# Kernel tuning notes

Hardware: AMD Instinct MI355X
Metric: run time of the kernel (lower is better)

## Reference

```python
import jax, jax.numpy as jnp
import numpy as np

E = 1024
BUCKET = 16
TAU = 0.75
ITERS = 8
SCALE = E ** -0.5
EPS = 1e-6


def _gumbel(rng, shape):
    u = jax.random.uniform(rng, shape, jnp.float32, 0.0, 1.0)
    return -jnp.log(-jnp.log(u + EPS) + EPS)


def _log_sinkhorn(log_alpha, n_iter):
    def body(i, la):
        la = la - jax.scipy.special.logsumexp(la, axis=-1, keepdims=True)
        la = la - jax.scipy.special.logsumexp(la, axis=-2, keepdims=True)
        return la
    return jnp.exp(jax.lax.fori_loop(0, n_iter, body, log_alpha))


def setup_inputs() -> dict:
    rng = jax.random.key(0)
    ks = jax.random.split(rng, 9)
    T, B, S = 4096, 8, 4096
    w = 0.02
    return {
        "query": jax.random.normal(ks[0], (T, B, E), jnp.float32),
        "key": jax.random.normal(ks[1], (S, B, E), jnp.float32),
        "value": jax.random.normal(ks[2], (S, B, E), jnp.float32),
        "wq": jax.random.normal(ks[3], (E, E), jnp.float32) * w,
        "bq": jnp.zeros((E,), jnp.float32),
        "wk": jax.random.normal(ks[4], (E, E), jnp.float32) * w,
        "bk": jnp.zeros((E,), jnp.float32),
        "wo": jax.random.normal(ks[5], (E, E), jnp.float32) * w,
        "bo": jnp.zeros((E,), jnp.float32),
    }


def reference(query, key, value, wq, bq, wk, bk, wo, bo):
    T, B, _ = query.shape
    S = key.shape[0]
    # projections (Linear: x @ W.T + b), move to (B, T, E)
    q = jnp.einsum('tbe,fe->btf', query, wq) + bq
    k = jnp.einsum('sbe,fe->bsf', key, wk) + bk
    v = jnp.transpose(value, (1, 0, 2))  # (B, S, E)
    nb, nkb = T // BUCKET, S // BUCKET
    # bucket aggregation: mean-pool q/k, flatten v buckets
    qb = q.reshape(B, nb, BUCKET, E).mean(axis=2)          # (B, nb, E)
    kb = k.reshape(B, nkb, BUCKET, E).mean(axis=2)         # (B, nkb, E)
    vb = v.reshape(B, nkb, BUCKET * E)                     # (B, nkb, BUCKET*E)
    # dot energy
    logits = jnp.einsum('bqe,bke->bqk', qb, kb) * SCALE    # (B, nb, nkb)
    log_alpha = logits
    # gumbel-sinkhorn (noise=True)
    g = _gumbel(jax.random.key(42), logits.shape)
    attn_weights = _log_sinkhorn((logits.astype(jnp.float32) + g) / TAU, ITERS)
    # attend on flattened buckets, then un-aggregate
    attn = jnp.einsum('bqk,bkd->bqd', attn_weights, vb)    # (B, nb, BUCKET*E)
    attn = attn.reshape(B, nb * BUCKET, E)
    attn = jnp.transpose(attn, (1, 0, 2))                  # (T, B, E)
    out = jnp.einsum('tbe,fe->tbf', attn, wo) + bo
    return out, attn_weights, log_alpha
```

## Files before the change

### kernel.cpp

```cpp
#include <hip/hip_runtime.h>


typedef float    f32x4 __attribute__((ext_vector_type(4)));
typedef _Float16 h4    __attribute__((ext_vector_type(4)));
typedef _Float16 h8    __attribute__((ext_vector_type(8)));

#define OUT_ELEMS 33554432
#define AW_ELEMS  524288

__device__ __forceinline__ void gload16(const void* g, void* l) {
  __builtin_amdgcn_global_load_lds((__attribute__((address_space(1))) void*)g,
                                   (__attribute__((address_space(3))) void*)l,
                                   16, 0, 0);
}

__global__ __launch_bounds__(256) void cb_k(const float* __restrict__ wq,
                                            const float* __restrict__ wk,
                                            const float* __restrict__ wo,
                                            _Float16* __restrict__ wdst,
                                            const float* __restrict__ q,
                                            const float* __restrict__ k,
                                            _Float16* __restrict__ qbar,
                                            _Float16* __restrict__ kbar) {
  __shared__ __attribute__((aligned(16))) float ldsbuf[16384];
  int bid = blockIdx.x;
  int tid = threadIdx.x;
  if (bid < 3072) {
    int which = bid >> 10;
    const float* src = which == 0 ? wq : (which == 1 ? wk : wo);
    size_t idx = (size_t)(bid & 1023) * 256 + tid;
    f32x4 v = ((const f32x4*)src)[idx];
    ((h4*)(wdst + (size_t)which * 1048576))[idx] = __builtin_convertvector(v, h4);
  } else {
    int vb = bid - 3072;
    int srcid = vb >> 11;
    int rem = vb & 2047;
    int i = rem >> 3;
    int b = (rem + i) & 7;
    const float* s2 = srcid ? k : q;
    _Float16* d2 = srcid ? kbar : qbar;
    const int w = tid >> 6;
    #pragma unroll
    for (int j = 0; j < 16; ++j) {
      int row = (i * 16 + j) * 8 + b;
      gload16(s2 + (size_t)row * 1024 + tid * 4, &ldsbuf[j * 1024 + w * 256]);
    }
    __syncthreads();
    const f32x4* l4 = (const f32x4*)ldsbuf;
    f32x4 a = {0.f, 0.f, 0.f, 0.f};
    #pragma unroll
    for (int j = 0; j < 16; ++j) a += l4[j * 256 + tid];
    a *= 0.0625f;
    ((h4*)(d2 + (size_t)(b * 256 + i) * 1024))[tid] = __builtin_convertvector(a, h4);
  }
}

__device__ __forceinline__ unsigned rotl32(unsigned x, int r) {
  return (x << r) | (x >> (32 - r));
}
__global__ __launch_bounds__(256) void gumbel_k(const float* __restrict__ logits,
                                                float* __restrict__ ebuf) {
  unsigned i = blockIdx.x * 256 + threadIdx.x;
  const unsigned k0 = 0u, k1 = 42u, k2 = 0u ^ 42u ^ 0x1BD11BDAu;
  unsigned x0 = 0u + k0, x1 = i + k1;
#define R4(a,b,c,d) \
  x0 += x1; x1 = rotl32(x1, a); x1 ^= x0; \
  x0 += x1; x1 = rotl32(x1, b); x1 ^= x0; \
  x0 += x1; x1 = rotl32(x1, c); x1 ^= x0; \
  x0 += x1; x1 = rotl32(x1, d); x1 ^= x0;
  R4(13,15,26,6)  x0 += k1; x1 += k2 + 1u;
  R4(17,29,16,24) x0 += k2; x1 += k0 + 2u;
  R4(13,15,26,6)  x0 += k0; x1 += k1 + 3u;
  R4(17,29,16,24) x0 += k1; x1 += k2 + 4u;
  R4(13,15,26,6)  x0 += k2; x1 += k0 + 5u;
#undef R4
  unsigned bits = x0 ^ x1;
  float u = __builtin_bit_cast(float, (bits >> 9) | 0x3f800000u) - 1.0f;
  float g = -logf(-logf(u + 1e-6f) + 1e-6f);
  ebuf[i] = __expf((logits[i] + g) / 0.75f);
}

__global__ __launch_bounds__(1024) void sinkvt_k(const float* __restrict__ ein,
                                                 float* __restrict__ attnw,
                                                 _Float16* __restrict__ wsh,
                                                 const float* __restrict__ v,
                                                 _Float16* __restrict__ vt) {
  __shared__ __attribute__((aligned(16))) char smem[36864];
  const int t = threadIdx.x;
  if (blockIdx.x < 8) {
    const int b = blockIdx.x;
    const int r = t >> 2, p = t & 3;
    const int k = t & 255, g = t >> 8;
    const float* Eb = ein + (size_t)b * 65536;
    const f32x4* Eb4 = (const f32x4*)Eb;
    float* ra = (float*)smem;
    float* cb = ra + 256;
    float (*part)[256] = (float (*)[256])(cb + 256);
    if (t < 256) cb[t] = 1.0f;
    __syncthreads();
    const f32x4* cb4 = (const f32x4*)cb;

    for (int it = 0; it < 8; ++it) {
      float s = 0.f;
      #pragma unroll
      for (int i = 0; i < 16; ++i) {
        f32x4 e = Eb4[r * 64 + p * 16 + i];
        f32x4 c = cb4[p * 16 + i];
        f32x4 m = e * c;
        s += (m[0] + m[1]) + (m[2] + m[3]);
      }
      s += __shfl_xor(s, 1, 64);
      s += __shfl_xor(s, 2, 64);
      if (p == 0) ra[r] = 1.0f / s;
      __syncthreads();
      float s2 = 0.f;
      #pragma unroll 8
      for (int q2 = 0; q2 < 64; ++q2) {
        int row = g * 64 + q2;
        s2 += Eb[row * 256 + k] * ra[row];
      }
      part[g][k] = s2;
      __syncthreads();
      if (t < 256) {
        cb[t] = 1.0f / (part[0][t] + part[1][t] + part[2][t] + part[3][t]);
      }
      __syncthreads();
    }

    const float arow = ra[r];
    f32x4* aw = (f32x4*)(attnw + (size_t)b * 65536 + r * 256 + p * 64);
    h4* wh = (h4*)(wsh + (size_t)b * 65536 + r * 256 + p * 64);
    #pragma unroll
    for (int i = 0; i < 16; ++i) {
      f32x4 e = Eb4[r * 64 + p * 16 + i];
      f32x4 c = cb4[p * 16 + i];
      f32x4 w = e * c * arow;
      aw[i] = w;
      h4 hv;
      hv[0] = (_Float16)w[0]; hv[1] = (_Float16)w[1];
      hv[2] = (_Float16)w[2]; hv[3] = (_Float16)w[3];
      wh[i] = hv;
    }
  } else {
    const int s = t >> 8, t2 = t & 255;
    int bid = (blockIdx.x - 8) * 4 + s;
    _Float16 (*tile)[72] = (_Float16 (*)[72])(smem + s * 9216);
    int kb = bid & 3, eb = (bid >> 2) & 15, j = (bid >> 6) & 15;
    int b = ((bid >> 10) + (bid & 7)) & 7;
    int k0 = kb * 64, e0 = eb * 64;
    int r = t2 >> 2, qq = t2 & 3;
    const float* src = v + ((size_t)((k0 + r) * 16 + j) * 8 + b) * 1024 + e0;
    #pragma unroll
    for (int ii = 0; ii < 4; ++ii) {
      f32x4 x = ((const f32x4*)src)[qq + ii * 4];
      *(h4*)&tile[r][(qq + ii * 4) * 4] = __builtin_convertvector(x, h4);
    }
    __syncthreads();
    _Float16* dstp = vt + (((size_t)(b * 16 + j) * 1024 + e0 + r) * 256 + k0 + qq * 16);
    h8 o0, o1;
    #pragma unroll
    for (int kk = 0; kk < 8; ++kk) o0[kk] = tile[qq * 16 + kk][r];
    #pragma unroll
    for (int kk = 0; kk < 8; ++kk) o1[kk] = tile[qq * 16 + 8 + kk][r];
    *(h8*)dstp = o0;
    *(h8*)(dstp + 8) = o1;
  }
}

template <int MODE>
__global__ __launch_bounds__(256) void gemm128(const _Float16* __restrict__ A,
                                               const _Float16* __restrict__ B,
                                               const float* __restrict__ bias,
                                               const float* __restrict__ bias2,
                                               void* __restrict__ out0,
                                               int K, int lda, int ldb) {
  const int tid = threadIdx.x, lane = tid & 63, w = tid >> 6;
  int bx = blockIdx.x, by = blockIdx.y, bz = blockIdx.z;
  if constexpr (MODE == 0) {
    int wid = ((bx & 7) << 4) + (bx >> 3);
    by = wid & 7; bx = wid >> 3;
  }
  if constexpr (MODE == 2) {
    int wid = ((bx & 7) << 8) + (bx >> 3);
    bz = wid >> 4; by = (wid >> 1) & 7; bx = wid & 1;
  }
  if constexpr (MODE == 3) {
    int wid = ((bx & 7) << 8) + (bx >> 3);
    by = wid & 7; bx = wid >> 3;
  }
  const int m0 = bx * 128, n0 = by * 128;
  const _Float16* Ab = A;
  const _Float16* Bb = B;
  const float* bs = bias;
  if constexpr (MODE == 0) {
    Ab += (size_t)bz * 2097152;
    Bb += (size_t)bz * 1048576;
    if (bz) bs = bias2;
  }
  if constexpr (MODE == 1) { Ab += (size_t)bz * 262144; Bb += (size_t)bz * 262144; }
  if constexpr (MODE == 2) { Ab += (size_t)(bz >> 4) * 65536; Bb += (size_t)bz * 262144; }
  __shared__ _Float16 lA[128 * 32];
  __shared__ _Float16 lB[128 * 32];
  f32x4 acc[4][4] = {};
  const int wm = (w >> 1) * 64, wn = (w & 1) * 64;
  const int fr = lane & 15, fk = (lane >> 4) * 8;
  const int q0 = tid, q1 = tid + 256;

  for (int kt = 0; kt < K; kt += 32) {
    __syncthreads();
    gload16(Ab + (size_t)(m0 + (q0 >> 2)) * lda + kt + (q0 & 3) * 8, &lA[(w * 64) * 8]);
    gload16(Ab + (size_t)(m0 + (q1 >> 2)) * lda + kt + (q1 & 3) * 8, &lA[(256 + w * 64) * 8]);
    gload16(Bb + (size_t)(n0 + (q0 >> 2)) * ldb + kt + (q0 & 3) * 8, &lB[(w * 64) * 8]);
    gload16(Bb + (size_t)(n0 + (q1 >> 2)) * ldb + kt + (q1 & 3) * 8, &lB[(256 + w * 64) * 8]);
    __syncthreads();
    h8 af[4], bf[4];
    #pragma unroll
    for (int i = 0; i < 4; ++i) {
      af[i] = *(const h8*)&lA[(wm + i * 16 + fr) * 32 + fk];
      bf[i] = *(const h8*)&lB[(wn + i * 16 + fr) * 32 + fk];
    }
    #pragma unroll
    for (int mi = 0; mi < 4; ++mi)
      #pragma unroll
      for (int ni = 0; ni < 4; ++ni)
        acc[mi][ni] = __builtin_amdgcn_mfma_f32_16x16x32_f16(af[mi], bf[ni], acc[mi][ni], 0, 0, 0);
  }

  const int er = (lane >> 4) * 4;
  #pragma unroll
  for (int mi = 0; mi < 4; ++mi) {
    #pragma unroll
    for (int ni = 0; ni < 4; ++ni) {
      #pragma unroll
      for (int r = 0; r < 4; ++r) {
        int row = m0 + wm + mi * 16 + er + r;
        int col = n0 + wn + ni * 16 + fr;
        float val = acc[mi][ni][r];
        if constexpr (MODE == 0) {
          ((_Float16*)out0)[(size_t)bz * 2097152 + (size_t)row * 1024 + col] =
              (_Float16)(val + bs[col]);
        } else if constexpr (MODE == 1) {
          ((float*)out0)[(size_t)bz * 65536 + row * 256 + col] = val * 0.03125f;
        } else if constexpr (MODE == 2) {
          int b = bz >> 4, j = bz & 15;
          ((_Float16*)out0)[((size_t)(b * 4096 + row * 16 + j)) * 1024 + col] = (_Float16)val;
        } else {
          int bb = row >> 12, t = row & 4095;
          ((float*)out0)[((size_t)t * 8 + bb) * 1024 + col] = val + bs[col];
        }
      }
    }
  }
}

extern "C" void kernel_launch(void* const* d_in, const int* in_sizes, int n_in,
                              void* d_out, int out_size, void* d_ws, size_t ws_size,
                              hipStream_t stream) {
  const float* query = (const float*)d_in[0];
  const float* key   = (const float*)d_in[1];
  const float* value = (const float*)d_in[2];
  const float* wq    = (const float*)d_in[3];
  const float* bq    = (const float*)d_in[4];
  const float* wk    = (const float*)d_in[5];
  const float* bk    = (const float*)d_in[6];
  const float* wo    = (const float*)d_in[7];
  const float* bo    = (const float*)d_in[8];

  float* out      = (float*)d_out;
  float* attnw    = out + OUT_ELEMS;
  float* logalpha = out + OUT_ELEMS + AW_ELEMS;

  char* ws = (char*)d_ws;
  const size_t MB = 1024 * 1024;
  _Float16* wqh   = (_Float16*)(ws + 0 * MB);
  _Float16* woh   = (_Float16*)(ws + 4 * MB);
  _Float16* qbar  = (_Float16*)(ws + 6 * MB);
  _Float16* kbar  = (_Float16*)(ws + 10 * MB);
  _Float16* qbh   = (_Float16*)(ws + 14 * MB);
  _Float16* kbh   = (_Float16*)(ws + 18 * MB);
  float*    ebuf  = (float*)(ws + 22 * MB);
  _Float16* wsh   = (_Float16*)(ws + 25 * MB);
  _Float16* vt    = (_Float16*)(ws + 26 * MB);
  _Float16* attnh = (_Float16*)(ws + 90 * MB);
  (void)in_sizes; (void)n_in; (void)out_size; (void)ws_size;

  cb_k<<<dim3(7168), 256, 0, stream>>>(wq, wk, wo, wqh, query, key, qbar, kbar);

  gemm128<0><<<dim3(128, 1, 2), 256, 0, stream>>>(qbar, wqh, bq, bk, qbh, 1024, 1024, 1024);
  gemm128<1><<<dim3(2, 2, 8), 256, 0, stream>>>(qbh, kbh, nullptr, nullptr, logalpha, 1024, 1024, 1024);

  gumbel_k<<<dim3(2048), 256, 0, stream>>>(logalpha, ebuf);
  sinkvt_k<<<dim3(2056), 1024, 0, stream>>>(ebuf, attnw, wsh, value, vt);

  gemm128<2><<<dim3(2048), 256, 0, stream>>>(wsh, vt, nullptr, nullptr, attnh, 256, 256, 256);
  gemm128<3><<<dim3(2048), 256, 0, stream>>>(attnh, woh, bo, nullptr, out, 1024, 1024, 1024);
}
```

Before: 345.9 us.

## Replace output projection GEMM with 256x256-tile double-buffered MFMA kernel

The final output projection (32768x1024x1024) moves from the generic 128x128 gemm to a dedicated 512-thread kernel with 256x256 tiles and a K-step of 64. Operands are staged with global_load_lds into a double buffer in 128KB of dynamic LDS, and the wait counts and barriers are arranged so the next tile's loads overlap the MFMA work. The larger tile raises arithmetic intensity and cuts global traffic per FLOP, at the cost of one block per CU, fewer blocks (512), and possible LDS bank conflicts from the unpadded layout.

```diff
diff --git a/kernel.cpp b/kernel.cpp
--- a/kernel.cpp
+++ b/kernel.cpp
@@ -184,10 +184,6 @@
     int wid = ((bx & 7) << 8) + (bx >> 3);
     bz = wid >> 4; by = (wid >> 1) & 7; bx = wid & 1;
   }
-  if constexpr (MODE == 3) {
-    int wid = ((bx & 7) << 8) + (bx >> 3);
-    by = wid & 7; bx = wid >> 3;
-  }
   const int m0 = bx * 128, n0 = by * 128;
   const _Float16* Ab = A;
   const _Float16* Bb = B;
@@ -241,13 +237,98 @@
               (_Float16)(val + bs[col]);
         } else if constexpr (MODE == 1) {
           ((float*)out0)[(size_t)bz * 65536 + row * 256 + col] = val * 0.03125f;
-        } else if constexpr (MODE == 2) {
+        } else {
           int b = bz >> 4, j = bz & 15;
           ((_Float16*)out0)[((size_t)(b * 4096 + row * 16 + j)) * 1024 + col] = (_Float16)val;
-        } else {
-          int bb = row >> 12, t = row & 4095;
-          ((float*)out0)[((size_t)t * 8 + bb) * 1024 + col] = val + bs[col];
         }
+      }
+    }
+  }
+}
+
+__global__ __launch_bounds__(512, 1) void gemm256_out(const _Float16* __restrict__ A,
+                                                      const _Float16* __restrict__ B,
+                                                      const float* __restrict__ bias,
+                                                      float* __restrict__ out) {
+  extern __shared__ __align__(16) _Float16 dsm[];
+  _Float16 (*lA)[16384] = (_Float16 (*)[16384])dsm;
+  _Float16 (*lB)[16384] = (_Float16 (*)[16384])(dsm + 32768);
+  const int tid = threadIdx.x, lane = tid & 63, w = tid >> 6;
+  const int wr = w >> 2, wc = w & 3;
+  int bx = blockIdx.x;
+  int wid = ((bx & 7) << 6) + (bx >> 3);
+  const int m0 = (wid >> 2) * 256, n0 = (wid & 3) * 256;
+  const int fr = lane & 15, fk = (lane >> 4) * 8;
+  f32x4 acc[8][4] = {};
+
+#define STAGE(t, buf) { \
+    const _Float16* Ag = A + (size_t)(m0 + (tid >> 3)) * 1024 + (t) * 64 + (tid & 7) * 8; \
+    const _Float16* Bg = B + (size_t)(n0 + (tid >> 3)) * 1024 + (t) * 64 + (tid & 7) * 8; \
+    _Float16* la0 = &lA[buf][w * 512]; \
+    _Float16* lb0 = &lB[buf][w * 512]; \
+    gload16(Ag,               la0); \
+    gload16(Ag +  64 * 1024,  la0 + 4096); \
+    gload16(Ag + 128 * 1024,  la0 + 8192); \
+    gload16(Ag + 192 * 1024,  la0 + 12288); \
+    gload16(Bg,               lb0); \
+    gload16(Bg +  64 * 1024,  lb0 + 4096); \
+    gload16(Bg + 128 * 1024,  lb0 + 8192); \
+    gload16(Bg + 192 * 1024,  lb0 + 12288); \
+  }
+
+  STAGE(0, 0)
+  STAGE(1, 1)
+
+  for (int t = 0; t < 16; ++t) {
+    const int bt = t & 1;
+    if (t < 15) { asm volatile("s_waitcnt vmcnt(8)" ::: "memory"); }
+    else        { asm volatile("s_waitcnt vmcnt(0)" ::: "memory"); }
+    __builtin_amdgcn_s_barrier();
+    h8 a0[8], b0[4];
+    #pragma unroll
+    for (int mi = 0; mi < 8; ++mi)
+      a0[mi] = *(const h8*)&lA[bt][(wr * 128 + mi * 16 + fr) * 64 + fk];
+    #pragma unroll
+    for (int ni = 0; ni < 4; ++ni)
+      b0[ni] = *(const h8*)&lB[bt][(wc * 64 + ni * 16 + fr) * 64 + fk];
+    #pragma unroll
+    for (int mi = 0; mi < 8; ++mi)
+      #pragma unroll
+      for (int ni = 0; ni < 4; ++ni)
+        acc[mi][ni] = __builtin_amdgcn_mfma_f32_16x16x32_f16(a0[mi], b0[ni], acc[mi][ni], 0, 0, 0);
+    h8 a1[8], b1[4];
+    #pragma unroll
+    for (int mi = 0; mi < 8; ++mi)
+      a1[mi] = *(const h8*)&lA[bt][(wr * 128 + mi * 16 + fr) * 64 + 32 + fk];
+    #pragma unroll
+    for (int ni = 0; ni < 4; ++ni)
+      b1[ni] = *(const h8*)&lB[bt][(wc * 64 + ni * 16 + fr) * 64 + 32 + fk];
+    asm volatile("s_waitcnt lgkmcnt(0)" ::: "memory");
+    __builtin_amdgcn_sched_barrier(0);
+    __builtin_amdgcn_s_barrier();
+    if (t + 2 < 16) STAGE(t + 2, bt)
+    __builtin_amdgcn_sched_barrier(0);
+    __builtin_amdgcn_s_setprio(1);
+    #pragma unroll
+    for (int mi = 0; mi < 8; ++mi)
+      #pragma unroll
+      for (int ni = 0; ni < 4; ++ni)
+        acc[mi][ni] = __builtin_amdgcn_mfma_f32_16x16x32_f16(a1[mi], b1[ni], acc[mi][ni], 0, 0, 0);
+    __builtin_amdgcn_s_setprio(0);
+  }
+#undef STAGE
+
+  const int er = (lane >> 4) * 4;
+  #pragma unroll
+  for (int mi = 0; mi < 8; ++mi) {
+    #pragma unroll
+    for (int ni = 0; ni < 4; ++ni) {
+      #pragma unroll
+      for (int r = 0; r < 4; ++r) {
+        int row = m0 + wr * 128 + mi * 16 + er + r;
+        int col = n0 + wc * 64 + ni * 16 + fr;
+        int bb = row >> 12, tt = row & 4095;
+        out[((size_t)tt * 8 + bb) * 1024 + col] = acc[mi][ni][r] + bias[col];
       }
     }
   }
@@ -293,5 +374,5 @@
   sinkvt_k<<<dim3(2056), 1024, 0, stream>>>(ebuf, attnw, wsh, value, vt);
 
   gemm128<2><<<dim3(2048), 256, 0, stream>>>(wsh, vt, nullptr, nullptr, attnh, 256, 256, 256);
-  gemm128<3><<<dim3(2048), 256, 0, stream>>>(attnh, woh, bo, nullptr, out, 1024, 1024, 1024);
-}
+  gemm256_out<<<dim3(512), 512, 131072, stream>>>(attnh, woh, bo, out);
+}
```

Measured after the change: 348.8 us. Within noise of the previous version (+0.9%).
